# Performance work log

Hardware: AMD Instinct MI355X
Metric: run time of the kernel (lower is better)

## Reference

```python
import jax, jax.numpy as jnp
import numpy as np

B, S1, S2, D1, D2, F = 8, 2048, 2048, 512, 512, 256

def setup_inputs() -> dict:
    key = jax.random.key(0)
    ks = jax.random.split(key, 10)
    sc1 = 1.0 / np.sqrt(D1)
    sc2 = 1.0 / np.sqrt(D2)
    scf = 1.0 / np.sqrt(F)
    return {
        "feat1": jax.random.normal(ks[0], (B, S1, D1), jnp.float32),
        "feat2": jax.random.normal(ks[1], (B, S2, D2), jnp.float32),
        "Wq": jax.random.normal(ks[2], (D1, F), jnp.float32) * sc1,
        "bq": jnp.zeros((F,), jnp.float32),
        "Wk": jax.random.normal(ks[3], (D2, F), jnp.float32) * sc2,
        "bk": jnp.zeros((F,), jnp.float32),
        "Wv": jax.random.normal(ks[4], (D2, F), jnp.float32) * sc2,
        "bv": jnp.zeros((F,), jnp.float32),
        "Wfc": jax.random.normal(ks[5], (F, F), jnp.float32) * scf,
        "bfc": jnp.zeros((F,), jnp.float32),
    }

def reference(feat1, feat2, Wq, bq, Wk, bk, Wv, bv, Wfc, bfc):
    Q = jnp.einsum('bsd,df->bsf', feat1, Wq) + bq          # [B,S1,F]
    K = jnp.einsum('btd,df->btf', feat2, Wk) + bk          # [B,S2,F]
    V = jnp.einsum('btd,df->btf', feat2, Wv) + bv          # [B,S2,F]
    scores = jnp.einsum('bsf,btf->bst', Q, K) / jnp.sqrt(jnp.float32(K.shape[-1]))
    attn = jax.nn.softmax(scores, axis=-1)                 # [B,S1,S2]
    attn_out = jnp.einsum('bst,btf->bsf', attn, V)         # [B,S1,F]
    out = jnp.einsum('bsf,fg->bsg', attn_out, Wfc) + bfc   # [B,S1,F]
    return out
```

## Files before the change

kernel.cpp:

```cpp
#include <hip/hip_runtime.h>
#include <hip/hip_bf16.h>

#define B_ 8
#define S1_ 2048
#define S2_ 2048
#define D_ 512
#define F_ 256

typedef __attribute__((ext_vector_type(4))) float f32x4;
typedef __attribute__((ext_vector_type(8))) short s16x8;
typedef __attribute__((ext_vector_type(4))) short s16x4;

__device__ __forceinline__ short f2bf(float x) {
  union { float f; unsigned u; } v; v.f = x;
  unsigned r = v.u + 0x7fffu + ((v.u >> 16) & 1u);
  return (short)(r >> 16);
}

__device__ __forceinline__ int pk2bf(float a, float b) {
  union { __hip_bfloat162 h; int i; } u;
  u.h = __float22bfloat162_rn(make_float2(a, b));
  return u.i;
}

__device__ __forceinline__ void gll16(const short* g, short* l) {
  __builtin_amdgcn_global_load_lds(
      (const __attribute__((address_space(1))) void*)g,
      (__attribute__((address_space(3))) void*)l, 16, 0, 0);
}

__global__ __launch_bounds__(256) void wtrans_kernel(
    const float* __restrict__ Wq, const float* __restrict__ Wk,
    const float* __restrict__ Wv, const float* __restrict__ Wfc,
    short* __restrict__ Wqt, short* __restrict__ Wkt,
    short* __restrict__ Wvt, short* __restrict__ Wfct) {
  int y = blockIdx.y;
  const float* W; short* Wt; int D;
  if (y == 0)      { W = Wq;  Wt = Wqt;  D = 512; }
  else if (y == 1) { W = Wk;  Wt = Wkt;  D = 512; }
  else if (y == 2) { W = Wv;  Wt = Wvt;  D = 512; }
  else             { W = Wfc; Wt = Wfct; D = 256; }
  int tiles_d = D >> 6;
  int bx = blockIdx.x;
  if (bx >= tiles_d * 4) return;
  int d0 = (bx % tiles_d) * 64, f0 = (bx / tiles_d) * 64;

  __shared__ short Ts[64][68];
  int t = threadIdx.x;
  int r = t >> 2, c16 = (t & 3) * 16;
  {
    const float* src = W + (size_t)(d0 + r) * F_ + f0 + c16;
    f32x4 v0 = *(const f32x4*)(src);
    f32x4 v1 = *(const f32x4*)(src + 4);
    f32x4 v2 = *(const f32x4*)(src + 8);
    f32x4 v3 = *(const f32x4*)(src + 12);
    s16x8 s0, s1;
    ((int*)&s0)[0] = pk2bf(v0[0], v0[1]); ((int*)&s0)[1] = pk2bf(v0[2], v0[3]);
    ((int*)&s0)[2] = pk2bf(v1[0], v1[1]); ((int*)&s0)[3] = pk2bf(v1[2], v1[3]);
    ((int*)&s1)[0] = pk2bf(v2[0], v2[1]); ((int*)&s1)[1] = pk2bf(v2[2], v2[3]);
    ((int*)&s1)[2] = pk2bf(v3[0], v3[1]); ((int*)&s1)[3] = pk2bf(v3[2], v3[3]);
    *(s16x8*)(&Ts[r][c16]) = s0;
    *(s16x8*)(&Ts[r][c16 + 8]) = s1;
  }
  __syncthreads();
  {
    int fr = t >> 2, dc16 = (t & 3) * 16;
    s16x8 o0, o1;
    for (int j = 0; j < 8; ++j) o0[j] = Ts[dc16 + j][fr];
    for (int j = 0; j < 8; ++j) o1[j] = Ts[dc16 + 8 + j][fr];
    short* dst = Wt + (size_t)(f0 + fr) * D + d0 + dc16;
    *(s16x8*)dst = o0;
    *(s16x8*)(dst + 8) = o1;
  }
}

__global__ __launch_bounds__(256, 3) void proj_kernel(
    const float* __restrict__ feat1, const float* __restrict__ feat2,
    const short* __restrict__ Wqt, const short* __restrict__ Wkt,
    const short* __restrict__ Wvt,
    const float* __restrict__ bq, const float* __restrict__ bk,
    const float* __restrict__ bv,
    short* __restrict__ Qw, short* __restrict__ Kw, short* __restrict__ Vtw) {
  const float* A; const short* Wt; const float* bias; short* outp;
  float scale; int trans;
  if (blockIdx.y == 0)      { A = feat1; Wt = Wqt; bias = bq; outp = Qw;  scale = 0.0625f; trans = 0; }
  else if (blockIdx.y == 1) { A = feat2; Wt = Wkt; bias = bk; outp = Kw;  scale = 1.0f;    trans = 0; }
  else                      { A = feat2; Wt = Wvt; bias = bv; outp = Vtw; scale = 1.0f;    trans = 1; }

  __shared__ __align__(16) short As[64][72];
  __shared__ __align__(16) short Ws[256][72];

  int m0 = blockIdx.x * 64;
  int t = threadIdx.x;
  int w = t >> 6, L = t & 63, rowA = L & 15, quad = L >> 4;
  int ar = t >> 2, ac16 = (t & 3) * 16;

  f32x4 acc[4][4];
  for (int i = 0; i < 4; ++i)
    for (int j = 0; j < 4; ++j) acc[i][j] = (f32x4){0.f, 0.f, 0.f, 0.f};

  for (int k0 = 0; k0 < D_; k0 += 64) {
    {
      const float* src = A + (size_t)(m0 + ar) * D_ + k0 + ac16;
      f32x4 v0 = *(const f32x4*)(src);
      f32x4 v1 = *(const f32x4*)(src + 4);
      f32x4 v2 = *(const f32x4*)(src + 8);
      f32x4 v3 = *(const f32x4*)(src + 12);
      s16x8 s0, s1;
      ((int*)&s0)[0] = pk2bf(v0[0], v0[1]); ((int*)&s0)[1] = pk2bf(v0[2], v0[3]);
      ((int*)&s0)[2] = pk2bf(v1[0], v1[1]); ((int*)&s0)[3] = pk2bf(v1[2], v1[3]);
      ((int*)&s1)[0] = pk2bf(v2[0], v2[1]); ((int*)&s1)[1] = pk2bf(v2[2], v2[3]);
      ((int*)&s1)[2] = pk2bf(v3[0], v3[1]); ((int*)&s1)[3] = pk2bf(v3[2], v3[3]);
      *(s16x8*)(&As[ar][ac16]) = s0;
      *(s16x8*)(&As[ar][ac16 + 8]) = s1;
    }
    for (int p = 0; p < 4; ++p) {
      int r = (t >> 2) + p * 64;
      const short* src = Wt + (size_t)r * D_ + k0 + ac16;
      *(s16x8*)(&Ws[r][ac16]) = *(const s16x8*)(src);
      *(s16x8*)(&Ws[r][ac16 + 8]) = *(const s16x8*)(src + 8);
    }
    __syncthreads();
    for (int kt = 0; kt < 2; ++kt) {
      s16x8 a[4];
      for (int mt = 0; mt < 4; ++mt)
        a[mt] = *(const s16x8*)(&As[mt * 16 + rowA][kt * 32 + quad * 8]);
      for (int nt = 0; nt < 4; ++nt) {
        s16x8 bfr = *(const s16x8*)(&Ws[w * 64 + nt * 16 + rowA][kt * 32 + quad * 8]);
        for (int mt = 0; mt < 4; ++mt)
          acc[mt][nt] = __builtin_amdgcn_mfma_f32_16x16x32_bf16(a[mt], bfr, acc[mt][nt], 0, 0, 0);
      }
    }
    __syncthreads();
  }

  if (!trans) {
    float bn[4];
    for (int nt = 0; nt < 4; ++nt) bn[nt] = bias[w * 64 + nt * 16 + rowA];
    for (int mt = 0; mt < 4; ++mt) {
      int m = m0 + mt * 16 + quad * 4;
      for (int nt = 0; nt < 4; ++nt) {
        int n = w * 64 + nt * 16 + rowA;
        for (int r = 0; r < 4; ++r)
          outp[(size_t)(m + r) * F_ + n] = f2bf((acc[mt][nt][r] + bn[nt]) * scale);
      }
    }
  } else {
    int bb = m0 >> 11;
    int tbase = m0 & (S2_ - 1);
    float bn[4];
    for (int nt = 0; nt < 4; ++nt) bn[nt] = bias[w * 64 + nt * 16 + rowA];
    for (int nt = 0; nt < 4; ++nt) {
      int f = w * 64 + nt * 16 + rowA;
      for (int mt = 0; mt < 4; ++mt) {
        int tt = tbase + mt * 16 + quad * 4;
        s16x4 o;
        for (int r = 0; r < 4; ++r) o[r] = f2bf(acc[mt][nt][r] + bn[nt]);
        *(s16x4*)(outp + ((size_t)bb * F_ + f) * S2_ + tt) = o;
      }
    }
  }
}

__global__ __launch_bounds__(512, 2) void flash_kernel(
    const short* __restrict__ Q,
    const short* __restrict__ K,
    const short* __restrict__ Vt,
    const short* __restrict__ Wfct,
    const float* __restrict__ bfc,
    float* __restrict__ out) {
  __shared__ __align__(16) short Ks[2][64][256];
  __shared__ __align__(16) short Vs[2][256][64];
  __shared__ __align__(16) short Ps[2][64][72];
  __shared__ float lf[128];

  int b = blockIdx.x & 7;
  int s0 = (blockIdx.x >> 3) * 64;
  int t = threadIdx.x;
  int w = t >> 6, L = t & 63, rowA = L & 15, quad = L >> 4;
  int isS = (w < 4);

  const short* Kb = K + (size_t)b * S2_ * F_;
  const short* Vb = Vt + (size_t)b * F_ * S2_;

  int rs = (w & 1) * 32, cs = ((w >> 1) & 1) * 32;
  int kxor = (rowA & 7) << 4;

  s16x8 qf[2][8];
  if (isS) {
    const short* Qb = Q + ((size_t)b * S1_ + s0 + rs) * F_;
    for (int mt = 0; mt < 2; ++mt)
      for (int kt = 0; kt < 8; ++kt)
        qf[mt][kt] = *(const s16x8*)(Qb + (size_t)(mt * 16 + rowA) * F_ + kt * 32 + quad * 8);
  }
  f32x4 o[4][4];
  for (int i = 0; i < 4; ++i)
    for (int j = 0; j < 4; ++j) o[i][j] = (f32x4){0.f, 0.f, 0.f, 0.f};
  float l_lane[2][4] = {{0.f,0.f,0.f,0.f},{0.f,0.f,0.f,0.f}};

  {
    int vL5 = L >> 5, vc = L & 31;
#pragma unroll
    for (int j = 0; j < 4; ++j) {
      int row = 8 * w + 2 * j + vL5;
      const short* src = Kb + (size_t)row * F_ + ((vc ^ (row & 7)) << 3);
      gll16(src, &Ks[0][8 * w + 2 * j][0]);
    }
  }

  for (int it = 0; it <= 32; ++it) {
    int cb = it & 1;
    __syncthreads();
    if (it < 32) {
      int vn0 = it << 6;
      int vL3 = L >> 3, vxor = ((L & 7) ^ ((L >> 3) & 7)) << 3;
#pragma unroll
      for (int j = 0; j < 4; ++j) {
        int row = 32 * w + 8 * j + vL3;
        const short* src = Vb + (size_t)row * S2_ + vn0 + vxor;
        gll16(src, &Vs[cb][32 * w + 8 * j][0]);
      }
      if (it < 31) {
        int kn0 = (it + 1) << 6;
        int kL5 = L >> 5, kc = L & 31;
#pragma unroll
        for (int j = 0; j < 4; ++j) {
          int row = 8 * w + 2 * j + kL5;
          const short* src = Kb + (size_t)(kn0 + row) * F_ + ((kc ^ (row & 7)) << 3);
          gll16(src, &Ks[1 - cb][8 * w + 2 * j][0]);
        }
      }
    }
    if (isS) {
      if (it < 32) {
        f32x4 s[2][2];
        for (int i = 0; i < 2; ++i)
          for (int j = 0; j < 2; ++j) s[i][j] = (f32x4){0.f, 0.f, 0.f, 0.f};
        const char* kb0 = (const char*)&Ks[cb][0][0] + ((size_t)(cs + rowA) << 9);
        const char* kb1 = kb0 + (16 << 9);
#pragma unroll
        for (int kt = 0; kt < 8; ++kt) {
          int off = (kt * 64 + quad * 16) ^ kxor;
          s16x8 bf0 = *(const s16x8*)(kb0 + off);
          s16x8 bf1 = *(const s16x8*)(kb1 + off);
          for (int mt = 0; mt < 2; ++mt) {
            s[mt][0] = __builtin_amdgcn_mfma_f32_16x16x32_bf16(qf[mt][kt], bf0, s[mt][0], 0, 0, 0);
            s[mt][1] = __builtin_amdgcn_mfma_f32_16x16x32_bf16(qf[mt][kt], bf1, s[mt][1], 0, 0, 0);
          }
        }
        for (int mt = 0; mt < 2; ++mt)
          for (int nt = 0; nt < 2; ++nt)
            for (int r = 0; r < 4; ++r) {
              float p = __expf(s[mt][nt][r]);
              l_lane[mt][r] += p;
              Ps[cb][rs + mt * 16 + quad * 4 + r][cs + nt * 16 + rowA] = f2bf(p);
            }
      }
    } else {
      if (it > 0) {
        int pb = 1 - cb;
        s16x8 pa[4][2];
#pragma unroll
        for (int mt = 0; mt < 4; ++mt)
          for (int kt = 0; kt < 2; ++kt)
            pa[mt][kt] = *(const s16x8*)(&Ps[pb][mt * 16 + rowA][kt * 32 + quad * 8]);
        const char* vb0 = (const char*)&Vs[pb][0][0] + (size_t)((w - 4) * 64 + rowA) * 128;
#pragma unroll
        for (int ft = 0; ft < 4; ++ft)
          for (int kt = 0; kt < 2; ++kt) {
            int off = (kt * 64 + quad * 16) ^ kxor;
            s16x8 vf = *(const s16x8*)(vb0 + (size_t)(ft * 16) * 128 + off);
            for (int mt = 0; mt < 4; ++mt)
              o[mt][ft] = __builtin_amdgcn_mfma_f32_16x16x32_bf16(pa[mt][kt], vf, o[mt][ft], 0, 0, 0);
          }
      }
    }
  }

  if (isS) {
    for (int mt = 0; mt < 2; ++mt)
      for (int r = 0; r < 4; ++r) {
        float x = l_lane[mt][r];
        for (int off = 1; off < 16; off <<= 1)
          x += __shfl_xor(x, off, 64);
        if (rowA == 0)
          lf[((w >> 1) & 1) * 64 + rs + mt * 16 + quad * 4 + r] = x;
      }
  }
  __syncthreads();

  short (*Olds)[264] = (short (*)[264])(&Ks[0][0][0]);
  if (!isS) {
    int fgc = (w - 4) * 64;
    for (int mt = 0; mt < 4; ++mt)
      for (int r = 0; r < 4; ++r) {
        int row = mt * 16 + quad * 4 + r;
        float inv = 1.0f / (lf[row] + lf[64 + row]);
        for (int ft = 0; ft < 4; ++ft)
          Olds[row][fgc + ft * 16 + rowA] = f2bf(o[mt][ft][r] * inv);
      }
  }
  __syncthreads();

  int mrow = (w & 3) * 16;
  int ng = (w >> 2) * 128;
  f32x4 fc[8];
  for (int i = 0; i < 8; ++i) fc[i] = (f32x4){0.f, 0.f, 0.f, 0.f};
#pragma unroll
  for (int kt = 0; kt < 8; ++kt) {
    s16x8 a = *(const s16x8*)(&Olds[mrow + rowA][kt * 32 + quad * 8]);
#pragma unroll
    for (int nt = 0; nt < 8; ++nt) {
      s16x8 bfr = *(const s16x8*)(Wfct + (size_t)(ng + nt * 16 + rowA) * 256 + kt * 32 + quad * 8);
      fc[nt] = __builtin_amdgcn_mfma_f32_16x16x32_bf16(a, bfr, fc[nt], 0, 0, 0);
    }
  }
  float* Ob = out + ((size_t)b * S1_ + s0) * F_;
#pragma unroll
  for (int nt = 0; nt < 8; ++nt) {
    int g = ng + nt * 16 + rowA;
    float bias = bfc[g];
#pragma unroll
    for (int r = 0; r < 4; ++r)
      Ob[(size_t)(mrow + quad * 4 + r) * F_ + g] = fc[nt][r] + bias;
  }
}

extern "C" void kernel_launch(void* const* d_in, const int* in_sizes, int n_in,
                              void* d_out, int out_size, void* d_ws, size_t ws_size,
                              hipStream_t stream) {
  const float* feat1 = (const float*)d_in[0];
  const float* feat2 = (const float*)d_in[1];
  const float* Wq  = (const float*)d_in[2];
  const float* bq  = (const float*)d_in[3];
  const float* Wk  = (const float*)d_in[4];
  const float* bk  = (const float*)d_in[5];
  const float* Wv  = (const float*)d_in[6];
  const float* bv  = (const float*)d_in[7];
  const float* Wfc = (const float*)d_in[8];
  const float* bfc = (const float*)d_in[9];
  float* out = (float*)d_out;
  char* ws = (char*)d_ws;

  short* Qw   = (short*)(ws);
  short* Kw   = (short*)(ws + (size_t)(8u  << 20));
  short* Vtw  = (short*)(ws + (size_t)(16u << 20));
  short* Wqt  = (short*)(ws + (size_t)(32u << 20));
  short* Wkt  = Wqt + 256 * 512;
  short* Wvt  = Wkt + 256 * 512;
  short* Wfct = Wvt + 256 * 512;

  wtrans_kernel<<<dim3(32, 4), 256, 0, stream>>>(Wq, Wk, Wv, Wfc, Wqt, Wkt, Wvt, Wfct);
  proj_kernel<<<dim3(256, 3), 256, 0, stream>>>(feat1, feat2, Wqt, Wkt, Wvt,
                                                bq, bk, bv, Qw, Kw, Vtw);
  flash_kernel<<<dim3(256), 512, 0, stream>>>(Qw, Kw, Vtw, Wfct, bfc, out);
}
```

Baseline: 200.9 us.

## Replace direct global-to-LDS loads with register-staged prefetch and padded LDS

Drops the global_load_lds path with XOR-swizzled layouts in the flash kernel. K and V tiles are now loaded into registers one to two iterations ahead and written to padded LDS arrays (row strides 264 and 72) that avoid bank conflicts without swizzling. This moves the copy through VGPRs, which raises register pressure under the 512-thread, 2-blocks-per-SM launch bound. It also adds LDS-store instructions in exchange for simpler addressing and deeper prefetch.

```diff
diff --git a/kernel.cpp b/kernel.cpp
--- a/kernel.cpp
+++ b/kernel.cpp
@@ -21,12 +21,6 @@
   union { __hip_bfloat162 h; int i; } u;
   u.h = __float22bfloat162_rn(make_float2(a, b));
   return u.i;
-}
-
-__device__ __forceinline__ void gll16(const short* g, short* l) {
-  __builtin_amdgcn_global_load_lds(
-      (const __attribute__((address_space(1))) void*)g,
-      (__attribute__((address_space(3))) void*)l, 16, 0, 0);
 }
 
 __global__ __launch_bounds__(256) void wtrans_kernel(
@@ -169,10 +163,10 @@
     const short* __restrict__ Wfct,
     const float* __restrict__ bfc,
     float* __restrict__ out) {
-  __shared__ __align__(16) short Ks[2][64][256];
-  __shared__ __align__(16) short Vs[2][256][64];
+  __shared__ __align__(16) short Ks[2][64][264];
+  __shared__ __align__(16) short Vs[2][256][72];
   __shared__ __align__(16) short Ps[2][64][72];
-  __shared__ float lf[128];
+  __shared__ float lfbuf[128];
 
   int b = blockIdx.x & 7;
   int s0 = (blockIdx.x >> 3) * 64;
@@ -183,8 +177,11 @@
   const short* Kb = K + (size_t)b * S2_ * F_;
   const short* Vb = Vt + (size_t)b * F_ * S2_;
 
+  int kr = t >> 5, kc8 = (t & 31) * 8;
+  int vr = t >> 3, vc8 = (t & 7) * 8;
+
   int rs = (w & 1) * 32, cs = ((w >> 1) & 1) * 32;
-  int kxor = (rowA & 7) << 4;
+  int fgc = (w - 4) * 64;
 
   s16x8 qf[2][8];
   if (isS) {
@@ -198,37 +195,33 @@
     for (int j = 0; j < 4; ++j) o[i][j] = (f32x4){0.f, 0.f, 0.f, 0.f};
   float l_lane[2][4] = {{0.f,0.f,0.f,0.f},{0.f,0.f,0.f,0.f}};
 
-  {
-    int vL5 = L >> 5, vc = L & 31;
-#pragma unroll
-    for (int j = 0; j < 4; ++j) {
-      int row = 8 * w + 2 * j + vL5;
-      const short* src = Kb + (size_t)row * F_ + ((vc ^ (row & 7)) << 3);
-      gll16(src, &Ks[0][8 * w + 2 * j][0]);
-    }
-  }
+  s16x8 kpre[4], vpre[4];
+  for (int p = 0; p < 4; ++p)
+    kpre[p] = *(const s16x8*)(Kb + (size_t)(kr + p * 16) * F_ + kc8);
+  for (int p = 0; p < 4; ++p)
+    *(s16x8*)(&Ks[0][kr + p * 16][kc8]) = kpre[p];
+  for (int p = 0; p < 4; ++p)
+    kpre[p] = *(const s16x8*)(Kb + (size_t)(64 + kr + p * 16) * F_ + kc8);
+  for (int p = 0; p < 4; ++p)
+    vpre[p] = *(const s16x8*)(Vb + (size_t)(vr + p * 64) * S2_ + vc8);
 
   for (int it = 0; it <= 32; ++it) {
     int cb = it & 1;
     __syncthreads();
     if (it < 32) {
-      int vn0 = it << 6;
-      int vL3 = L >> 3, vxor = ((L & 7) ^ ((L >> 3) & 7)) << 3;
-#pragma unroll
-      for (int j = 0; j < 4; ++j) {
-        int row = 32 * w + 8 * j + vL3;
-        const short* src = Vb + (size_t)row * S2_ + vn0 + vxor;
-        gll16(src, &Vs[cb][32 * w + 8 * j][0]);
-      }
+      for (int p = 0; p < 4; ++p)
+        *(s16x8*)(&Vs[cb][vr + p * 64][vc8]) = vpre[p];
       if (it < 31) {
-        int kn0 = (it + 1) << 6;
-        int kL5 = L >> 5, kc = L & 31;
-#pragma unroll
-        for (int j = 0; j < 4; ++j) {
-          int row = 8 * w + 2 * j + kL5;
-          const short* src = Kb + (size_t)(kn0 + row) * F_ + ((kc ^ (row & 7)) << 3);
-          gll16(src, &Ks[1 - cb][8 * w + 2 * j][0]);
-        }
+        for (int p = 0; p < 4; ++p)
+          *(s16x8*)(&Ks[1 - cb][kr + p * 16][kc8]) = kpre[p];
+        int n0 = (it + 1) * 64;
+        for (int p = 0; p < 4; ++p)
+          vpre[p] = *(const s16x8*)(Vb + (size_t)(vr + p * 64) * S2_ + n0 + vc8);
+      }
+      if (it < 30) {
+        int n0 = (it + 2) * 64;
+        for (int p = 0; p < 4; ++p)
+          kpre[p] = *(const s16x8*)(Kb + (size_t)(n0 + kr + p * 16) * F_ + kc8);
       }
     }
     if (isS) {
@@ -236,13 +229,9 @@
         f32x4 s[2][2];
         for (int i = 0; i < 2; ++i)
           for (int j = 0; j < 2; ++j) s[i][j] = (f32x4){0.f, 0.f, 0.f, 0.f};
-        const char* kb0 = (const char*)&Ks[cb][0][0] + ((size_t)(cs + rowA) << 9);
-        const char* kb1 = kb0 + (16 << 9);
-#pragma unroll
         for (int kt = 0; kt < 8; ++kt) {
-          int off = (kt * 64 + quad * 16) ^ kxor;
-          s16x8 bf0 = *(const s16x8*)(kb0 + off);
-          s16x8 bf1 = *(const s16x8*)(kb1 + off);
+          s16x8 bf0 = *(const s16x8*)(&Ks[cb][cs + rowA][kt * 32 + quad * 8]);
+          s16x8 bf1 = *(const s16x8*)(&Ks[cb][cs + 16 + rowA][kt * 32 + quad * 8]);
           for (int mt = 0; mt < 2; ++mt) {
             s[mt][0] = __builtin_amdgcn_mfma_f32_16x16x32_bf16(qf[mt][kt], bf0, s[mt][0], 0, 0, 0);
             s[mt][1] = __builtin_amdgcn_mfma_f32_16x16x32_bf16(qf[mt][kt], bf1, s[mt][1], 0, 0, 0);
@@ -264,12 +253,10 @@
         for (int mt = 0; mt < 4; ++mt)
           for (int kt = 0; kt < 2; ++kt)
             pa[mt][kt] = *(const s16x8*)(&Ps[pb][mt * 16 + rowA][kt * 32 + quad * 8]);
-        const char* vb0 = (const char*)&Vs[pb][0][0] + (size_t)((w - 4) * 64 + rowA) * 128;
 #pragma unroll
         for (int ft = 0; ft < 4; ++ft)
           for (int kt = 0; kt < 2; ++kt) {
-            int off = (kt * 64 + quad * 16) ^ kxor;
-            s16x8 vf = *(const s16x8*)(vb0 + (size_t)(ft * 16) * 128 + off);
+            s16x8 vf = *(const s16x8*)(&Vs[pb][fgc + ft * 16 + rowA][kt * 32 + quad * 8]);
             for (int mt = 0; mt < 4; ++mt)
               o[mt][ft] = __builtin_amdgcn_mfma_f32_16x16x32_bf16(pa[mt][kt], vf, o[mt][ft], 0, 0, 0);
           }
@@ -284,18 +271,17 @@
         for (int off = 1; off < 16; off <<= 1)
           x += __shfl_xor(x, off, 64);
         if (rowA == 0)
-          lf[((w >> 1) & 1) * 64 + rs + mt * 16 + quad * 4 + r] = x;
+          lfbuf[((w >> 1) & 1) * 64 + rs + mt * 16 + quad * 4 + r] = x;
       }
   }
   __syncthreads();
 
   short (*Olds)[264] = (short (*)[264])(&Ks[0][0][0]);
   if (!isS) {
-    int fgc = (w - 4) * 64;
     for (int mt = 0; mt < 4; ++mt)
       for (int r = 0; r < 4; ++r) {
         int row = mt * 16 + quad * 4 + r;
-        float inv = 1.0f / (lf[row] + lf[64 + row]);
+        float inv = 1.0f / (lfbuf[row] + lfbuf[64 + row]);
         for (int ft = 0; ft < 4; ++ft)
           Olds[row][fgc + ft * 16 + rowA] = f2bf(o[mt][ft][r] * inv);
       }
```

New measurement: 198.8 us. About the same (-1.1%).
